# Optimization experiments

Measured on AMD Instinct MI355X. Metric: run time of the kernel, lower is better.

## Reference

```python
import jax, jax.numpy as jnp
import numpy as np

N_NODES = 100000
D = 128


def gcn_conv(x, W, b, src, dst, deg_inv_sqrt):
    # PyG GCNConv: linear transform, symmetric-normalized aggregation with self-loops, bias
    h = x @ W  # [N, D_out]
    norm = deg_inv_sqrt[src] * deg_inv_sqrt[dst]  # [E_tot]
    msgs = h[src] * norm[:, None]  # gather + scale  [E_tot, D_out]
    out = jax.ops.segment_sum(msgs, dst, num_segments=x.shape[0])  # scatter-add to targets
    return out + b


def _prep_edges(edge_index, n_nodes):
    # add self-loops (weight 1) and compute deg^{-1/2} over targets (flow source_to_target)
    loops = jnp.arange(n_nodes, dtype=edge_index.dtype)
    src = jnp.concatenate([edge_index[0], loops])
    dst = jnp.concatenate([edge_index[1], loops])
    deg = jax.ops.segment_sum(jnp.ones_like(dst, dtype=jnp.float32), dst, num_segments=n_nodes)
    deg_inv_sqrt = jnp.where(deg > 0, jax.lax.rsqrt(jnp.maximum(deg, 1.0)), 0.0)
    return src, dst, deg_inv_sqrt


def setup_inputs() -> dict:
    key = jax.random.key(0)
    ks = jax.random.split(key, 8)
    node_fts = jax.random.normal(ks[0], (N_NODES, D), dtype=jnp.float32)
    edge_index = jax.random.randint(ks[1], (2, 1600000), 0, N_NODES, dtype=jnp.int64)
    scale = 1.0 / np.sqrt(D)
    W1 = jax.random.uniform(ks[2], (D, D), jnp.float32, -scale, scale)
    b1 = jnp.zeros((D,), jnp.float32)
    W2 = jax.random.uniform(ks[3], (D, D), jnp.float32, -scale, scale)
    b2 = jnp.zeros((D,), jnp.float32)
    W3 = jax.random.uniform(ks[4], (D, D), jnp.float32, -scale, scale)
    b3 = jnp.zeros((D,), jnp.float32)
    return {"node_fts": node_fts, "edge_index": edge_index,
            "W1": W1, "b1": b1, "W2": W2, "b2": b2, "W3": W3, "b3": b3}


def reference(node_fts, edge_index, W1, b1, W2, b2, W3, b3):
    n = node_fts.shape[0]
    src, dst, dinv = _prep_edges(edge_index, n)
    x = jax.nn.relu(gcn_conv(node_fts, W1, b1, src, dst, dinv))
    x = jax.nn.relu(gcn_conv(x, W2, b2, src, dst, dinv))
    x = jax.nn.relu(gcn_conv(x, W3, b3, src, dst, dinv))
    return x
```

## Files before the change

### kernel.cpp

```cpp
#include <hip/hip_runtime.h>

#define NN 100000
#define EE 1600000
#define D 128
#define NPART 8
#define PSZ (NN / NPART)
#define NI4 (EE / 4)
#define SUBW 196
#define NSB (NPART * 64)
#define SCAP 4096
#define RCAP 8192
#define LBCAP 96

typedef __attribute__((ext_vector_type(8))) short bf16x8;
typedef __attribute__((ext_vector_type(4))) float f32x4;

__device__ inline unsigned int f2bf2(float a, float b) {
    unsigned int ua = __float_as_uint(a);
    unsigned int ub = __float_as_uint(b);
    ua = (ua + 0x7fffu + ((ua >> 16) & 1u)) >> 16;
    ub = (ub + 0x7fffu + ((ub >> 16) & 1u)) >> 16;
    return ua | (ub << 16);
}
__device__ inline unsigned short f2bf(float a) {
    unsigned int u = __float_as_uint(a);
    return (unsigned short)((u + 0x7fffu + ((u >> 16) & 1u)) >> 16);
}
__device__ inline float2 bf2f2(unsigned int u) {
    return make_float2(__uint_as_float(u << 16), __uint_as_float(u & 0xffff0000u));
}


__global__ void init_kernel(int* __restrict__ gcur2, unsigned int* __restrict__ hb) {
    int i = blockIdx.x * blockDim.x + threadIdx.x;
    if (i < NSB) gcur2[i] = 0;
    if (i < 64) hb[(size_t)NN * 64 + i] = 0;
}

__global__ __launch_bounds__(256) void filterbin_kernel(const int4* __restrict__ src4,
                                                        const int4* __restrict__ dst4,
                                                        int* __restrict__ gcur2,
                                                        uint2* __restrict__ buckets2) {
    __shared__ uint2 bins[64][LBCAP];
    __shared__ int bcnt[64];
    __shared__ int gbase[64];
    const int p = blockIdx.x >> 6;
    const int c = blockIdx.x & 63;
    if (threadIdx.x < 64) bcnt[threadIdx.x] = 0;
    __syncthreads();
    const int lo = p * PSZ, hi = lo + PSZ;
    const int chunk4 = NI4 / 64;
    const int a0 = c * chunk4, a1 = a0 + chunk4;
    for (int i = a0 + threadIdx.x; i < a1; i += 256) {
        int4 d4 = dst4[i];
        bool m0 = (d4.x >= lo && d4.x < hi);
        bool m1 = (d4.y >= lo && d4.y < hi);
        bool m2 = (d4.z >= lo && d4.z < hi);
        bool m3 = (d4.w >= lo && d4.w < hi);
        if (!(m0 | m1 | m2 | m3)) continue;
        int4 s4 = src4[i];
        int ss[4] = {s4.x, s4.y, s4.z, s4.w};
        int dd[4] = {d4.x, d4.y, d4.z, d4.w};
        bool mm[4] = {m0, m1, m2, m3};
#pragma unroll
        for (int k = 0; k < 4; ++k) {
            if (!mm[k]) continue;
            int li = (dd[k] - lo) / SUBW;
            int pos = atomicAdd(&bcnt[li], 1);
            if (pos < LBCAP) {
                bins[li][pos] = make_uint2((unsigned)ss[k], (unsigned)dd[k]);
            } else {
                int sb = p * 64 + li;
                int gp = atomicAdd(&gcur2[sb], 1);
                buckets2[(size_t)sb * SCAP + gp] = make_uint2((unsigned)ss[k], (unsigned)dd[k]);
            }
        }
    }
    __syncthreads();
    if (threadIdx.x < 64) {
        int cc = min(bcnt[threadIdx.x], LBCAP);
        gbase[threadIdx.x] = atomicAdd(&gcur2[p * 64 + threadIdx.x], cc);
        bcnt[threadIdx.x] = cc;
    }
    __syncthreads();
    for (int b = 0; b < 64; ++b) {
        const int cc = bcnt[b];
        uint2* outp = buckets2 + (size_t)(p * 64 + b) * SCAP + gbase[b];
        for (int i = threadIdx.x; i < cc; i += 256) outp[i] = bins[b][i];
    }
}

__global__ __launch_bounds__(256) void sort3_kernel(const uint2* __restrict__ buckets2,
                                                    const int* __restrict__ gcur2,
                                                    int* __restrict__ csr,
                                                    int* __restrict__ info,
                                                    float* __restrict__ dinv) {
    __shared__ int hist[256];
    __shared__ int pscan[256];
    __shared__ int lcur[256];
    __shared__ int staged[RCAP];
    const int sb = blockIdx.x;
    const int li = sb & 63;
    const int base_node = (sb >> 6) * PSZ + li * SUBW;
    const int nnodes = min(SUBW, PSZ - li * SUBW);
    const int scnt = gcur2[sb];
    const uint2* bk = buckets2 + (size_t)sb * SCAP;
    const int t = threadIdx.x;
    hist[t] = 0;
    __syncthreads();
    for (int i = t; i < scnt; i += 256) atomicAdd(&hist[(int)bk[i].y - base_node], 1);
    __syncthreads();
    const int padded = (t < nnodes) ? ((hist[t] + 7) & ~7) : 0;
    pscan[t] = padded;
    __syncthreads();
    for (int off = 1; off < 256; off <<= 1) {
        int v = (t >= off) ? pscan[t - off] : 0;
        __syncthreads();
        pscan[t] += v;
        __syncthreads();
    }
    const int rstart = pscan[t] - padded;
    lcur[t] = rstart;
    __syncthreads();
    const int total = pscan[255];
    for (int i = t; i < total; i += 256) staged[i] = NN;
    __syncthreads();
    for (int i = t; i < scnt; i += 256) {
        uint2 r = bk[i];
        int pos = atomicAdd(&lcur[(int)r.y - base_node], 1);
        staged[pos] = (int)r.x;
    }
    __syncthreads();
    int4* co = (int4*)(csr + (size_t)sb * RCAP);
    for (int i = t; i < (total >> 2); i += 256) co[i] = ((const int4*)staged)[i];
    if (t < nnodes) {
        int dg = hist[t];
        info[base_node + t] = ((sb * RCAP + rstart) << 8) | dg;
        dinv[base_node + t] = rsqrtf(1.0f + (float)dg);
    }
}

__global__ void wt_build3_kernel(const float* __restrict__ W1, const float* __restrict__ W2,
                                 const float* __restrict__ W3, unsigned short* __restrict__ wt1,
                                 unsigned short* __restrict__ wt2, unsigned short* __restrict__ wt3) {
    const int which = blockIdx.x >> 6;
    const float* W = which == 0 ? W1 : (which == 1 ? W2 : W3);
    unsigned short* wt = which == 0 ? wt1 : (which == 1 ? wt2 : wt3);
    int i = (blockIdx.x & 63) * 256 + threadIdx.x;
    int n = i >> 7, k = i & 127;
    wt[n * 128 + k] = f2bf(W[k * 128 + n]);
}


template <bool F32IN>
__global__ __launch_bounds__(256) void gemm_mfma_kernel(const void* __restrict__ xin,
                                                        const unsigned short* __restrict__ wt,
                                                        const float* __restrict__ dinv,
                                                        unsigned int* __restrict__ hb) {
    const int wave = blockIdx.x * 4 + (threadIdx.x >> 6);
    const int m0 = wave * 16;
    if (m0 >= NN) return;
    const int lane = threadIdx.x & 63;
    const int r = lane & 15;
    const int q = lane >> 4;
    const unsigned short* wrow = wt + (size_t)r * 128 + q * 8;
    f32x4 acc[8] = {};
#pragma unroll
    for (int kc = 0; kc < 4; ++kc) {
        bf16x8 xf;
        if (F32IN) {
            const float* xrow = (const float*)xin + (size_t)(m0 + r) * 128 + q * 8 + kc * 32;
            float4 a = *(const float4*)xrow;
            float4 b = *(const float4*)(xrow + 4);
            unsigned short tmp[8] = {f2bf(a.x), f2bf(a.y), f2bf(a.z), f2bf(a.w),
                                     f2bf(b.x), f2bf(b.y), f2bf(b.z), f2bf(b.w)};
            xf = *(const bf16x8*)tmp;
        } else {
            const unsigned short* xrow =
                (const unsigned short*)xin + (size_t)(m0 + r) * 128 + q * 8 + kc * 32;
            xf = *(const bf16x8*)xrow;
        }
#pragma unroll
        for (int nt = 0; nt < 8; ++nt) {
            bf16x8 wf = *(const bf16x8*)(wrow + (size_t)nt * 16 * 128 + kc * 32);
            acc[nt] = __builtin_amdgcn_mfma_f32_16x16x32_bf16(wf, xf, acc[nt], 0, 0, 0);
        }
    }
    const float dvr = dinv[m0 + r];
    unsigned int* hrow = hb + (size_t)(m0 + r) * 64;
#pragma unroll
    for (int nt = 0; nt < 8; ++nt) {
        int n = nt * 16 + q * 4;
        *(uint2*)(hrow + (n >> 1)) =
            make_uint2(f2bf2(acc[nt][0] * dvr, acc[nt][1] * dvr),
                       f2bf2(acc[nt][2] * dvr, acc[nt][3] * dvr));
    }
}


template <bool BF16OUT>
__global__ __launch_bounds__(256) void aggregate_kernel(const unsigned int* __restrict__ hb,
                                                        const int* __restrict__ csr,
                                                        const int* __restrict__ info,
                                                        const float* __restrict__ dinv,
                                                        const float2* __restrict__ bias2,
                                                        void* __restrict__ outp) {
    const int d = blockIdx.x * 4 + (threadIdx.x >> 6);
    const int j = threadIdx.x & 63;
    const int ifo = info[d];
    int e = ifo >> 8;
    const int end = e + (((ifo & 255) + 7) & ~7);
    float2 acc = bf2f2(hb[(size_t)d * 64 + j]);
    for (; e + 16 <= end; e += 16) {
        int4 c0 = *(const int4*)(csr + e);
        int4 c1 = *(const int4*)(csr + e + 4);
        int4 c2 = *(const int4*)(csr + e + 8);
        int4 c3 = *(const int4*)(csr + e + 12);
        unsigned int v0 = hb[(size_t)c0.x * 64 + j];
        unsigned int v1 = hb[(size_t)c0.y * 64 + j];
        unsigned int v2 = hb[(size_t)c0.z * 64 + j];
        unsigned int v3 = hb[(size_t)c0.w * 64 + j];
        unsigned int v4 = hb[(size_t)c1.x * 64 + j];
        unsigned int v5 = hb[(size_t)c1.y * 64 + j];
        unsigned int v6 = hb[(size_t)c1.z * 64 + j];
        unsigned int v7 = hb[(size_t)c1.w * 64 + j];
        unsigned int v8 = hb[(size_t)c2.x * 64 + j];
        unsigned int v9 = hb[(size_t)c2.y * 64 + j];
        unsigned int va = hb[(size_t)c2.z * 64 + j];
        unsigned int vb = hb[(size_t)c2.w * 64 + j];
        unsigned int vc = hb[(size_t)c3.x * 64 + j];
        unsigned int vd = hb[(size_t)c3.y * 64 + j];
        unsigned int ve = hb[(size_t)c3.z * 64 + j];
        unsigned int vf = hb[(size_t)c3.w * 64 + j];
        float2 f0 = bf2f2(v0), f1 = bf2f2(v1), f2 = bf2f2(v2), f3 = bf2f2(v3);
        float2 f4 = bf2f2(v4), f5 = bf2f2(v5), f6 = bf2f2(v6), f7 = bf2f2(v7);
        float2 f8 = bf2f2(v8), f9 = bf2f2(v9), fa = bf2f2(va), fb = bf2f2(vb);
        float2 fc = bf2f2(vc), fd = bf2f2(vd), fe = bf2f2(ve), ff = bf2f2(vf);
        acc.x += ((f0.x + f1.x) + (f2.x + f3.x)) + ((f4.x + f5.x) + (f6.x + f7.x)) +
                 ((f8.x + f9.x) + (fa.x + fb.x)) + ((fc.x + fd.x) + (fe.x + ff.x));
        acc.y += ((f0.y + f1.y) + (f2.y + f3.y)) + ((f4.y + f5.y) + (f6.y + f7.y)) +
                 ((f8.y + f9.y) + (fa.y + fb.y)) + ((fc.y + fd.y) + (fe.y + ff.y));
    }
    if (e < end) {
        int4 c0 = *(const int4*)(csr + e);
        int4 c1 = *(const int4*)(csr + e + 4);
        unsigned int v0 = hb[(size_t)c0.x * 64 + j];
        unsigned int v1 = hb[(size_t)c0.y * 64 + j];
        unsigned int v2 = hb[(size_t)c0.z * 64 + j];
        unsigned int v3 = hb[(size_t)c0.w * 64 + j];
        unsigned int v4 = hb[(size_t)c1.x * 64 + j];
        unsigned int v5 = hb[(size_t)c1.y * 64 + j];
        unsigned int v6 = hb[(size_t)c1.z * 64 + j];
        unsigned int v7 = hb[(size_t)c1.w * 64 + j];
        float2 f0 = bf2f2(v0), f1 = bf2f2(v1), f2 = bf2f2(v2), f3 = bf2f2(v3);
        float2 f4 = bf2f2(v4), f5 = bf2f2(v5), f6 = bf2f2(v6), f7 = bf2f2(v7);
        acc.x += ((f0.x + f1.x) + (f2.x + f3.x)) + ((f4.x + f5.x) + (f6.x + f7.x));
        acc.y += ((f0.y + f1.y) + (f2.y + f3.y)) + ((f4.y + f5.y) + (f6.y + f7.y));
    }
    const float dv = dinv[d];
    float2 bb = bias2[j];
    float ox = fmaxf(dv * acc.x + bb.x, 0.0f);
    float oy = fmaxf(dv * acc.y + bb.y, 0.0f);
    if (BF16OUT) {
        ((unsigned int*)outp)[(size_t)d * 64 + j] = f2bf2(ox, oy);
    } else {
        ((float2*)outp)[(size_t)d * 64 + j] = make_float2(ox, oy);
    }
}


extern "C" void kernel_launch(void* const* d_in, const int* in_sizes, int n_in,
                              void* d_out, int out_size, void* d_ws, size_t ws_size,
                              hipStream_t stream) {
    const float* x0 = (const float*)d_in[0];
    const int* ei = (const int*)d_in[1];
    const float* W1 = (const float*)d_in[2];
    const float* b1 = (const float*)d_in[3];
    const float* W2 = (const float*)d_in[4];
    const float* b2 = (const float*)d_in[5];
    const float* W3 = (const float*)d_in[6];
    const float* b3 = (const float*)d_in[7];
    float* out = (float*)d_out;

    char* ws = (char*)d_ws;
    size_t off = 0;
    auto alloc = [&](size_t bytes) -> void* {
        off = (off + 511) & ~(size_t)511;
        void* p = ws + off;
        off += bytes;
        return p;
    };
    unsigned int* hb  = (unsigned int*)alloc(((size_t)NN + 1) * 64 * 4);
    int*   csr     = (int*)  alloc((size_t)NSB * RCAP * sizeof(int));
    uint2* buckets2 = (uint2*)alloc((size_t)NSB * SCAP * sizeof(uint2));
    int*   info    = (int*)  alloc((size_t)NN * sizeof(int));
    float* dinv    = (float*)alloc((size_t)NN * sizeof(float));
    int*   gcur2   = (int*)  alloc(NSB * sizeof(int));
    unsigned short* wt1 = (unsigned short*)alloc(128 * 128 * 2);
    unsigned short* wt2 = (unsigned short*)alloc(128 * 128 * 2);
    unsigned short* wt3 = (unsigned short*)alloc(128 * 128 * 2);

    unsigned int* xact = (unsigned int*)d_out;

    const int4* src4 = (const int4*)ei;
    const int4* dst4 = (const int4*)(ei + EE);

    init_kernel<<<2, 256, 0, stream>>>(gcur2, hb);
    filterbin_kernel<<<NSB, 256, 0, stream>>>(src4, dst4, gcur2, buckets2);
    sort3_kernel<<<NSB, 256, 0, stream>>>(buckets2, gcur2, csr, info, dinv);
    wt_build3_kernel<<<192, 256, 0, stream>>>(W1, W2, W3, wt1, wt2, wt3);

    const int gemmBlocks = (NN / 16 + 3) / 4;

    gemm_mfma_kernel<true><<<gemmBlocks, 256, 0, stream>>>((const void*)x0, wt1, dinv, hb);
    aggregate_kernel<true><<<NN / 4, 256, 0, stream>>>(hb, csr, info, dinv,
                                                       (const float2*)b1, (void*)xact);
    gemm_mfma_kernel<false><<<gemmBlocks, 256, 0, stream>>>((const void*)xact, wt2, dinv, hb);
    aggregate_kernel<true><<<NN / 4, 256, 0, stream>>>(hb, csr, info, dinv,
                                                       (const float2*)b2, (void*)xact);
    gemm_mfma_kernel<false><<<gemmBlocks, 256, 0, stream>>>((const void*)xact, wt3, dinv, hb);
    aggregate_kernel<false><<<NN / 4, 256, 0, stream>>>(hb, csr, info, dinv,
                                                        (const float2*)b3, (void*)out);
}
```

Measured before the change: 435.4 us.

## Reorder GCN to aggregate-then-transform and fuse aggregation with MFMA GEMM per layer

Uses linearity to aggregate the dinv-scaled input features first and then apply the weight matrix, fusing gather-aggregation and the MFMA GEMM into one kernel per layer via an LDS tile of 64 rows. This removes the separate GEMM launches and the hb intermediate round-trip through global memory. The next layer's dinv prescale is folded into the epilogue. Each block now handles 64 destinations with 4 waves doing 16 sequential gathers each, which cuts parallelism and latency hiding in the gather phase. It also rounds the aggregated sum to bf16 before the GEMM.

```diff
diff --git a/kernel.cpp b/kernel.cpp
--- a/kernel.cpp
+++ b/kernel.cpp
@@ -31,10 +31,14 @@
 }
 
 
-__global__ void init_kernel(int* __restrict__ gcur2, unsigned int* __restrict__ hb) {
+__global__ void init_kernel(int* __restrict__ gcur2, unsigned int* __restrict__ xsA,
+                            unsigned int* __restrict__ xsB) {
     int i = blockIdx.x * blockDim.x + threadIdx.x;
     if (i < NSB) gcur2[i] = 0;
-    if (i < 64) hb[(size_t)NN * 64 + i] = 0;
+    if (i < 64) {
+        xsA[(size_t)NN * 64 + i] = 0;
+        xsB[(size_t)NN * 64 + i] = 0;
+    }
 }
 
 __global__ __launch_bounds__(256) void filterbin_kernel(const int4* __restrict__ src4,
@@ -151,120 +155,131 @@
     wt[n * 128 + k] = f2bf(W[k * 128 + n]);
 }
 
-
-template <bool F32IN>
-__global__ __launch_bounds__(256) void gemm_mfma_kernel(const void* __restrict__ xin,
-                                                        const unsigned short* __restrict__ wt,
-                                                        const float* __restrict__ dinv,
-                                                        unsigned int* __restrict__ hb) {
-    const int wave = blockIdx.x * 4 + (threadIdx.x >> 6);
-    const int m0 = wave * 16;
-    if (m0 >= NN) return;
-    const int lane = threadIdx.x & 63;
-    const int r = lane & 15;
-    const int q = lane >> 4;
+__global__ __launch_bounds__(256) void scale0_kernel(const float* __restrict__ x0,
+                                                     const float* __restrict__ dinv,
+                                                     unsigned int* __restrict__ xs) {
+    int i = blockIdx.x * 256 + threadIdx.x;
+    int row = i >> 5, c = (i & 31) * 4;
+    float4 v = *(const float4*)(x0 + (size_t)row * 128 + c);
+    float dv = dinv[row];
+    *(uint2*)(xs + (size_t)row * 64 + (c >> 1)) =
+        make_uint2(f2bf2(v.x * dv, v.y * dv), f2bf2(v.z * dv, v.w * dv));
+}
+
+
+template <bool LAST>
+__global__ __launch_bounds__(256) void fused_kernel(const unsigned int* __restrict__ xs,
+                                                    const unsigned short* __restrict__ wt,
+                                                    const int* __restrict__ csr,
+                                                    const int* __restrict__ info,
+                                                    const float* __restrict__ dinv,
+                                                    const float* __restrict__ bias,
+                                                    void* __restrict__ outp) {
+    __shared__ unsigned int ylds[64 * 68];
+    const int w = threadIdx.x >> 6;
+    const int j = threadIdx.x & 63;
+    const int base = blockIdx.x * 64;
+
+    for (int i = 0; i < 16; ++i) {
+        const int d = base + w * 16 + i;
+        if (d >= NN) break;
+        const int ifo = info[d];
+        int e = ifo >> 8;
+        const int end = e + (((ifo & 255) + 7) & ~7);
+        float2 acc = bf2f2(xs[(size_t)d * 64 + j]);
+        for (; e + 16 <= end; e += 16) {
+            int4 c0 = *(const int4*)(csr + e);
+            int4 c1 = *(const int4*)(csr + e + 4);
+            int4 c2 = *(const int4*)(csr + e + 8);
+            int4 c3 = *(const int4*)(csr + e + 12);
+            unsigned int v0 = xs[(size_t)c0.x * 64 + j];
+            unsigned int v1 = xs[(size_t)c0.y * 64 + j];
+            unsigned int v2 = xs[(size_t)c0.z * 64 + j];
+            unsigned int v3 = xs[(size_t)c0.w * 64 + j];
+            unsigned int v4 = xs[(size_t)c1.x * 64 + j];
+            unsigned int v5 = xs[(size_t)c1.y * 64 + j];
+            unsigned int v6 = xs[(size_t)c1.z * 64 + j];
+            unsigned int v7 = xs[(size_t)c1.w * 64 + j];
+            unsigned int v8 = xs[(size_t)c2.x * 64 + j];
+            unsigned int v9 = xs[(size_t)c2.y * 64 + j];
+            unsigned int va = xs[(size_t)c2.z * 64 + j];
+            unsigned int vb = xs[(size_t)c2.w * 64 + j];
+            unsigned int vc = xs[(size_t)c3.x * 64 + j];
+            unsigned int vd = xs[(size_t)c3.y * 64 + j];
+            unsigned int ve = xs[(size_t)c3.z * 64 + j];
+            unsigned int vf = xs[(size_t)c3.w * 64 + j];
+            float2 f0 = bf2f2(v0), f1 = bf2f2(v1), f2 = bf2f2(v2), f3 = bf2f2(v3);
+            float2 f4 = bf2f2(v4), f5 = bf2f2(v5), f6 = bf2f2(v6), f7 = bf2f2(v7);
+            float2 f8 = bf2f2(v8), f9 = bf2f2(v9), fa = bf2f2(va), fb = bf2f2(vb);
+            float2 fc = bf2f2(vc), fd = bf2f2(vd), fe = bf2f2(ve), ff = bf2f2(vf);
+            acc.x += ((f0.x + f1.x) + (f2.x + f3.x)) + ((f4.x + f5.x) + (f6.x + f7.x)) +
+                     ((f8.x + f9.x) + (fa.x + fb.x)) + ((fc.x + fd.x) + (fe.x + ff.x));
+            acc.y += ((f0.y + f1.y) + (f2.y + f3.y)) + ((f4.y + f5.y) + (f6.y + f7.y)) +
+                     ((f8.y + f9.y) + (fa.y + fb.y)) + ((fc.y + fd.y) + (fe.y + ff.y));
+        }
+        if (e < end) {
+            int4 c0 = *(const int4*)(csr + e);
+            int4 c1 = *(const int4*)(csr + e + 4);
+            unsigned int v0 = xs[(size_t)c0.x * 64 + j];
+            unsigned int v1 = xs[(size_t)c0.y * 64 + j];
+            unsigned int v2 = xs[(size_t)c0.z * 64 + j];
+            unsigned int v3 = xs[(size_t)c0.w * 64 + j];
+            unsigned int v4 = xs[(size_t)c1.x * 64 + j];
+            unsigned int v5 = xs[(size_t)c1.y * 64 + j];
+            unsigned int v6 = xs[(size_t)c1.z * 64 + j];
+            unsigned int v7 = xs[(size_t)c1.w * 64 + j];
+            float2 f0 = bf2f2(v0), f1 = bf2f2(v1), f2 = bf2f2(v2), f3 = bf2f2(v3);
+            float2 f4 = bf2f2(v4), f5 = bf2f2(v5), f6 = bf2f2(v6), f7 = bf2f2(v7);
+            acc.x += ((f0.x + f1.x) + (f2.x + f3.x)) + ((f4.x + f5.x) + (f6.x + f7.x));
+            acc.y += ((f0.y + f1.y) + (f2.y + f3.y)) + ((f4.y + f5.y) + (f6.y + f7.y));
+        }
+        const float dv = dinv[d];
+        ylds[(w * 16 + i) * 68 + j] = f2bf2(dv * acc.x, dv * acc.y);
+    }
+    __syncthreads();
+
+    const int r = j & 15;
+    const int q = j >> 4;
     const unsigned short* wrow = wt + (size_t)r * 128 + q * 8;
+    const int myrow = w * 16 + r;
     f32x4 acc[8] = {};
 #pragma unroll
     for (int kc = 0; kc < 4; ++kc) {
-        bf16x8 xf;
-        if (F32IN) {
-            const float* xrow = (const float*)xin + (size_t)(m0 + r) * 128 + q * 8 + kc * 32;
-            float4 a = *(const float4*)xrow;
-            float4 b = *(const float4*)(xrow + 4);
-            unsigned short tmp[8] = {f2bf(a.x), f2bf(a.y), f2bf(a.z), f2bf(a.w),
-                                     f2bf(b.x), f2bf(b.y), f2bf(b.z), f2bf(b.w)};
-            xf = *(const bf16x8*)tmp;
-        } else {
-            const unsigned short* xrow =
-                (const unsigned short*)xin + (size_t)(m0 + r) * 128 + q * 8 + kc * 32;
-            xf = *(const bf16x8*)xrow;
-        }
+        bf16x8 xf = *(const bf16x8*)(ylds + myrow * 68 + q * 4 + kc * 16);
 #pragma unroll
         for (int nt = 0; nt < 8; ++nt) {
             bf16x8 wf = *(const bf16x8*)(wrow + (size_t)nt * 16 * 128 + kc * 32);
             acc[nt] = __builtin_amdgcn_mfma_f32_16x16x32_bf16(wf, xf, acc[nt], 0, 0, 0);
         }
     }
-    const float dvr = dinv[m0 + r];
-    unsigned int* hrow = hb + (size_t)(m0 + r) * 64;
-#pragma unroll
-    for (int nt = 0; nt < 8; ++nt) {
-        int n = nt * 16 + q * 4;
-        *(uint2*)(hrow + (n >> 1)) =
-            make_uint2(f2bf2(acc[nt][0] * dvr, acc[nt][1] * dvr),
-                       f2bf2(acc[nt][2] * dvr, acc[nt][3] * dvr));
-    }
-}
-
-
-template <bool BF16OUT>
-__global__ __launch_bounds__(256) void aggregate_kernel(const unsigned int* __restrict__ hb,
-                                                        const int* __restrict__ csr,
-                                                        const int* __restrict__ info,
-                                                        const float* __restrict__ dinv,
-                                                        const float2* __restrict__ bias2,
-                                                        void* __restrict__ outp) {
-    const int d = blockIdx.x * 4 + (threadIdx.x >> 6);
-    const int j = threadIdx.x & 63;
-    const int ifo = info[d];
-    int e = ifo >> 8;
-    const int end = e + (((ifo & 255) + 7) & ~7);
-    float2 acc = bf2f2(hb[(size_t)d * 64 + j]);
-    for (; e + 16 <= end; e += 16) {
-        int4 c0 = *(const int4*)(csr + e);
-        int4 c1 = *(const int4*)(csr + e + 4);
-        int4 c2 = *(const int4*)(csr + e + 8);
-        int4 c3 = *(const int4*)(csr + e + 12);
-        unsigned int v0 = hb[(size_t)c0.x * 64 + j];
-        unsigned int v1 = hb[(size_t)c0.y * 64 + j];
-        unsigned int v2 = hb[(size_t)c0.z * 64 + j];
-        unsigned int v3 = hb[(size_t)c0.w * 64 + j];
-        unsigned int v4 = hb[(size_t)c1.x * 64 + j];
-        unsigned int v5 = hb[(size_t)c1.y * 64 + j];
-        unsigned int v6 = hb[(size_t)c1.z * 64 + j];
-        unsigned int v7 = hb[(size_t)c1.w * 64 + j];
-        unsigned int v8 = hb[(size_t)c2.x * 64 + j];
-        unsigned int v9 = hb[(size_t)c2.y * 64 + j];
-        unsigned int va = hb[(size_t)c2.z * 64 + j];
-        unsigned int vb = hb[(size_t)c2.w * 64 + j];
-        unsigned int vc = hb[(size_t)c3.x * 64 + j];
-        unsigned int vd = hb[(size_t)c3.y * 64 + j];
-        unsigned int ve = hb[(size_t)c3.z * 64 + j];
-        unsigned int vf = hb[(size_t)c3.w * 64 + j];
-        float2 f0 = bf2f2(v0), f1 = bf2f2(v1), f2 = bf2f2(v2), f3 = bf2f2(v3);
-        float2 f4 = bf2f2(v4), f5 = bf2f2(v5), f6 = bf2f2(v6), f7 = bf2f2(v7);
-        float2 f8 = bf2f2(v8), f9 = bf2f2(v9), fa = bf2f2(va), fb = bf2f2(vb);
-        float2 fc = bf2f2(vc), fd = bf2f2(vd), fe = bf2f2(ve), ff = bf2f2(vf);
-        acc.x += ((f0.x + f1.x) + (f2.x + f3.x)) + ((f4.x + f5.x) + (f6.x + f7.x)) +
-                 ((f8.x + f9.x) + (fa.x + fb.x)) + ((fc.x + fd.x) + (fe.x + ff.x));
-        acc.y += ((f0.y + f1.y) + (f2.y + f3.y)) + ((f4.y + f5.y) + (f6.y + f7.y)) +
-                 ((f8.y + f9.y) + (fa.y + fb.y)) + ((fc.y + fd.y) + (fe.y + ff.y));
-    }
-    if (e < end) {
-        int4 c0 = *(const int4*)(csr + e);
-        int4 c1 = *(const int4*)(csr + e + 4);
-        unsigned int v0 = hb[(size_t)c0.x * 64 + j];
-        unsigned int v1 = hb[(size_t)c0.y * 64 + j];
-        unsigned int v2 = hb[(size_t)c0.z * 64 + j];
-        unsigned int v3 = hb[(size_t)c0.w * 64 + j];
-        unsigned int v4 = hb[(size_t)c1.x * 64 + j];
-        unsigned int v5 = hb[(size_t)c1.y * 64 + j];
-        unsigned int v6 = hb[(size_t)c1.z * 64 + j];
-        unsigned int v7 = hb[(size_t)c1.w * 64 + j];
-        float2 f0 = bf2f2(v0), f1 = bf2f2(v1), f2 = bf2f2(v2), f3 = bf2f2(v3);
-        float2 f4 = bf2f2(v4), f5 = bf2f2(v5), f6 = bf2f2(v6), f7 = bf2f2(v7);
-        acc.x += ((f0.x + f1.x) + (f2.x + f3.x)) + ((f4.x + f5.x) + (f6.x + f7.x));
-        acc.y += ((f0.y + f1.y) + (f2.y + f3.y)) + ((f4.y + f5.y) + (f6.y + f7.y));
-    }
-    const float dv = dinv[d];
-    float2 bb = bias2[j];
-    float ox = fmaxf(dv * acc.x + bb.x, 0.0f);
-    float oy = fmaxf(dv * acc.y + bb.y, 0.0f);
-    if (BF16OUT) {
-        ((unsigned int*)outp)[(size_t)d * 64 + j] = f2bf2(ox, oy);
+    const int orow = base + myrow;
+    if (orow >= NN) return;
+    if (LAST) {
+        float* op = (float*)outp + (size_t)orow * 128;
+#pragma unroll
+        for (int nt = 0; nt < 8; ++nt) {
+            int n = nt * 16 + q * 4;
+            float4 bb = *(const float4*)(bias + n);
+            float4 o;
+            o.x = fmaxf(acc[nt][0] + bb.x, 0.0f);
+            o.y = fmaxf(acc[nt][1] + bb.y, 0.0f);
+            o.z = fmaxf(acc[nt][2] + bb.z, 0.0f);
+            o.w = fmaxf(acc[nt][3] + bb.w, 0.0f);
+            *(float4*)(op + n) = o;
+        }
     } else {
-        ((float2*)outp)[(size_t)d * 64 + j] = make_float2(ox, oy);
+        const float dvr = dinv[orow];
+        unsigned int* op = (unsigned int*)outp + (size_t)orow * 64;
+#pragma unroll
+        for (int nt = 0; nt < 8; ++nt) {
+            int n = nt * 16 + q * 4;
+            float4 bb = *(const float4*)(bias + n);
+            float o0 = fmaxf(acc[nt][0] + bb.x, 0.0f) * dvr;
+            float o1 = fmaxf(acc[nt][1] + bb.y, 0.0f) * dvr;
+            float o2 = fmaxf(acc[nt][2] + bb.z, 0.0f) * dvr;
+            float o3 = fmaxf(acc[nt][3] + bb.w, 0.0f) * dvr;
+            *(uint2*)(op + (n >> 1)) = make_uint2(f2bf2(o0, o1), f2bf2(o2, o3));
+        }
     }
 }
 
@@ -290,7 +305,7 @@
         off += bytes;
         return p;
     };
-    unsigned int* hb  = (unsigned int*)alloc(((size_t)NN + 1) * 64 * 4);
+    unsigned int* xsA = (unsigned int*)alloc(((size_t)NN + 1) * 64 * 4);
     int*   csr     = (int*)  alloc((size_t)NSB * RCAP * sizeof(int));
     uint2* buckets2 = (uint2*)alloc((size_t)NSB * SCAP * sizeof(uint2));
     int*   info    = (int*)  alloc((size_t)NN * sizeof(int));
@@ -300,25 +315,20 @@
     unsigned short* wt2 = (unsigned short*)alloc(128 * 128 * 2);
     unsigned short* wt3 = (unsigned short*)alloc(128 * 128 * 2);
 
-    unsigned int* xact = (unsigned int*)d_out;
+    unsigned int* xsB = (unsigned int*)d_out;
 
     const int4* src4 = (const int4*)ei;
     const int4* dst4 = (const int4*)(ei + EE);
 
-    init_kernel<<<2, 256, 0, stream>>>(gcur2, hb);
+    init_kernel<<<2, 256, 0, stream>>>(gcur2, xsA, xsB);
     filterbin_kernel<<<NSB, 256, 0, stream>>>(src4, dst4, gcur2, buckets2);
     sort3_kernel<<<NSB, 256, 0, stream>>>(buckets2, gcur2, csr, info, dinv);
     wt_build3_kernel<<<192, 256, 0, stream>>>(W1, W2, W3, wt1, wt2, wt3);
-
-    const int gemmBlocks = (NN / 16 + 3) / 4;
-
-    gemm_mfma_kernel<true><<<gemmBlocks, 256, 0, stream>>>((const void*)x0, wt1, dinv, hb);
-    aggregate_kernel<true><<<NN / 4, 256, 0, stream>>>(hb, csr, info, dinv,
-                                                       (const float2*)b1, (void*)xact);
-    gemm_mfma_kernel<false><<<gemmBlocks, 256, 0, stream>>>((const void*)xact, wt2, dinv, hb);
-    aggregate_kernel<true><<<NN / 4, 256, 0, stream>>>(hb, csr, info, dinv,
-                                                       (const float2*)b2, (void*)xact);
-    gemm_mfma_kernel<false><<<gemmBlocks, 256, 0, stream>>>((const void*)xact, wt3, dinv, hb);
-    aggregate_kernel<false><<<NN / 4, 256, 0, stream>>>(hb, csr, info, dinv,
-                                                        (const float2*)b3, (void*)out);
-}
+    scale0_kernel<<<NN * 32 / 256, 256, 0, stream>>>(x0, dinv, xsA);
+
+    const int fusedBlocks = (NN + 63) / 64;
+
+    fused_kernel<false><<<fusedBlocks, 256, 0, stream>>>(xsA, wt1, csr, info, dinv, b1, (void*)xsB);
+    fused_kernel<false><<<fusedBlocks, 256, 0, stream>>>(xsB, wt2, csr, info, dinv, b2, (void*)xsA);
+    fused_kernel<true><<<fusedBlocks, 256, 0, stream>>>(xsA, wt3, csr, info, dinv, b3, (void*)out);
+}
```

New measurement: 462.2 us. 1.06x slower.

## Fuse weight prep into binning, overlap sort with first GEMM, register-cache weights

Applied to the files above, without the earlier changes.

Folds the weight transpose/convert and hb sentinel init into extra blocks of the edge binning kernel, and replaces the init kernel with memsets. Degree is counted via global atomics during binning, so the first GEMM can compute dinv itself and run as extra blocks inside the sort kernel instead of as a separate launch. GEMM waves now keep all weight fragments in registers and process four 16-row tiles each, cutting repeated weight loads. The cost is one global atomic per edge, higher register pressure, and a fixed grid split within the fused kernels.

```diff
diff --git a/kernel.cpp b/kernel.cpp
--- a/kernel.cpp
+++ b/kernel.cpp
@@ -31,16 +31,27 @@
 }
 
 
-__global__ void init_kernel(int* __restrict__ gcur2, unsigned int* __restrict__ hb) {
-    int i = blockIdx.x * blockDim.x + threadIdx.x;
-    if (i < NSB) gcur2[i] = 0;
-    if (i < 64) hb[(size_t)NN * 64 + i] = 0;
-}
-
-__global__ __launch_bounds__(256) void filterbin_kernel(const int4* __restrict__ src4,
-                                                        const int4* __restrict__ dst4,
-                                                        int* __restrict__ gcur2,
-                                                        uint2* __restrict__ buckets2) {
+__global__ __launch_bounds__(256) void fbwt_kernel(const int4* __restrict__ src4,
+                                                   const int4* __restrict__ dst4,
+                                                   int* __restrict__ gcur2,
+                                                   uint2* __restrict__ buckets2,
+                                                   int* __restrict__ deg,
+                                                   const float* __restrict__ W1,
+                                                   const float* __restrict__ W2,
+                                                   const float* __restrict__ W3,
+                                                   unsigned short* __restrict__ wt1,
+                                                   unsigned short* __restrict__ wt2,
+                                                   unsigned short* __restrict__ wt3,
+                                                   unsigned int* __restrict__ hb) {
+    if (blockIdx.x >= 512) {
+        const int g = (blockIdx.x - 512) * 256 + threadIdx.x;
+        const int n = g >> 7, k = g & 127;
+        wt1[n * 128 + k] = f2bf(W1[k * 128 + n]);
+        wt2[n * 128 + k] = f2bf(W2[k * 128 + n]);
+        wt3[n * 128 + k] = f2bf(W3[k * 128 + n]);
+        if (blockIdx.x == 512 && threadIdx.x < 64) hb[(size_t)NN * 64 + threadIdx.x] = 0;
+        return;
+    }
     __shared__ uint2 bins[64][LBCAP];
     __shared__ int bcnt[64];
     __shared__ int gbase[64];
@@ -65,6 +76,7 @@
 #pragma unroll
         for (int k = 0; k < 4; ++k) {
             if (!mm[k]) continue;
+            atomicAdd(&deg[dd[k]], 1);
             int li = (dd[k] - lo) / SUBW;
             int pos = atomicAdd(&bcnt[li], 1);
             if (pos < LBCAP) {
@@ -90,15 +102,80 @@
     }
 }
 
-__global__ __launch_bounds__(256) void sort3_kernel(const uint2* __restrict__ buckets2,
-                                                    const int* __restrict__ gcur2,
-                                                    int* __restrict__ csr,
-                                                    int* __restrict__ info,
-                                                    float* __restrict__ dinv) {
+
+template <bool F32IN>
+__device__ __forceinline__ void gemm_body(int wave, const void* __restrict__ xin,
+                                          const unsigned short* __restrict__ wt,
+                                          const int* __restrict__ deg,
+                                          unsigned int* __restrict__ hb) {
+    const int base = wave * 64;
+    if (base >= NN) return;
+    const int lane = threadIdx.x & 63;
+    const int r = lane & 15;
+    const int q = lane >> 4;
+    const unsigned short* wrow = wt + (size_t)r * 128 + q * 8;
+    bf16x8 wfr[4][8];
+#pragma unroll
+    for (int kc = 0; kc < 4; ++kc)
+#pragma unroll
+        for (int nt = 0; nt < 8; ++nt)
+            wfr[kc][nt] = *(const bf16x8*)(wrow + (size_t)nt * 16 * 128 + kc * 32);
+#pragma unroll
+    for (int tt = 0; tt < 4; ++tt) {
+        const int m0 = base + tt * 16;
+        if (m0 >= NN) break;
+        f32x4 acc[8] = {};
+#pragma unroll
+        for (int kc = 0; kc < 4; ++kc) {
+            bf16x8 xf;
+            if (F32IN) {
+                const float* xrow = (const float*)xin + (size_t)(m0 + r) * 128 + q * 8 + kc * 32;
+                float4 a = *(const float4*)xrow;
+                float4 b = *(const float4*)(xrow + 4);
+                unsigned short tmp[8] = {f2bf(a.x), f2bf(a.y), f2bf(a.z), f2bf(a.w),
+                                         f2bf(b.x), f2bf(b.y), f2bf(b.z), f2bf(b.w)};
+                xf = *(const bf16x8*)tmp;
+            } else {
+                const unsigned short* xrow =
+                    (const unsigned short*)xin + (size_t)(m0 + r) * 128 + q * 8 + kc * 32;
+                xf = *(const bf16x8*)xrow;
+            }
+#pragma unroll
+            for (int nt = 0; nt < 8; ++nt)
+                acc[nt] = __builtin_amdgcn_mfma_f32_16x16x32_bf16(wfr[kc][nt], xf, acc[nt], 0, 0, 0);
+        }
+        const int orow = m0 + r;
+        const float dvr = rsqrtf(1.0f + (float)deg[orow]);
+        unsigned int* hrow = hb + (size_t)orow * 64;
+#pragma unroll
+        for (int nt = 0; nt < 8; ++nt) {
+            int n = nt * 16 + q * 4;
+            *(uint2*)(hrow + (n >> 1)) =
+                make_uint2(f2bf2(acc[nt][0] * dvr, acc[nt][1] * dvr),
+                           f2bf2(acc[nt][2] * dvr, acc[nt][3] * dvr));
+        }
+    }
+}
+
+
+__global__ __launch_bounds__(256, 2) void sort3_gemm1_kernel(const uint2* __restrict__ buckets2,
+                                                             const int* __restrict__ gcur2,
+                                                             int* __restrict__ csr,
+                                                             int* __restrict__ info,
+                                                             float* __restrict__ dinv,
+                                                             const float* __restrict__ x0,
+                                                             const unsigned short* __restrict__ wt1,
+                                                             const int* __restrict__ deg,
+                                                             unsigned int* __restrict__ hb) {
     __shared__ int hist[256];
     __shared__ int pscan[256];
     __shared__ int lcur[256];
     __shared__ int staged[RCAP];
+    if (blockIdx.x >= 512) {
+        const int wave = (blockIdx.x - 512) * 4 + (threadIdx.x >> 6);
+        gemm_body<true>(wave, (const void*)x0, wt1, deg, hb);
+        return;
+    }
     const int sb = blockIdx.x;
     const int li = sb & 63;
     const int base_node = (sb >> 6) * PSZ + li * SUBW;
@@ -140,61 +217,13 @@
     }
 }
 
-__global__ void wt_build3_kernel(const float* __restrict__ W1, const float* __restrict__ W2,
-                                 const float* __restrict__ W3, unsigned short* __restrict__ wt1,
-                                 unsigned short* __restrict__ wt2, unsigned short* __restrict__ wt3) {
-    const int which = blockIdx.x >> 6;
-    const float* W = which == 0 ? W1 : (which == 1 ? W2 : W3);
-    unsigned short* wt = which == 0 ? wt1 : (which == 1 ? wt2 : wt3);
-    int i = (blockIdx.x & 63) * 256 + threadIdx.x;
-    int n = i >> 7, k = i & 127;
-    wt[n * 128 + k] = f2bf(W[k * 128 + n]);
-}
-
-
 template <bool F32IN>
-__global__ __launch_bounds__(256) void gemm_mfma_kernel(const void* __restrict__ xin,
-                                                        const unsigned short* __restrict__ wt,
-                                                        const float* __restrict__ dinv,
-                                                        unsigned int* __restrict__ hb) {
+__global__ __launch_bounds__(256, 2) void gemm_kernel(const void* __restrict__ xin,
+                                                      const unsigned short* __restrict__ wt,
+                                                      const int* __restrict__ deg,
+                                                      unsigned int* __restrict__ hb) {
     const int wave = blockIdx.x * 4 + (threadIdx.x >> 6);
-    const int m0 = wave * 16;
-    if (m0 >= NN) return;
-    const int lane = threadIdx.x & 63;
-    const int r = lane & 15;
-    const int q = lane >> 4;
-    const unsigned short* wrow = wt + (size_t)r * 128 + q * 8;
-    f32x4 acc[8] = {};
-#pragma unroll
-    for (int kc = 0; kc < 4; ++kc) {
-        bf16x8 xf;
-        if (F32IN) {
-            const float* xrow = (const float*)xin + (size_t)(m0 + r) * 128 + q * 8 + kc * 32;
-            float4 a = *(const float4*)xrow;
-            float4 b = *(const float4*)(xrow + 4);
-            unsigned short tmp[8] = {f2bf(a.x), f2bf(a.y), f2bf(a.z), f2bf(a.w),
-                                     f2bf(b.x), f2bf(b.y), f2bf(b.z), f2bf(b.w)};
-            xf = *(const bf16x8*)tmp;
-        } else {
-            const unsigned short* xrow =
-                (const unsigned short*)xin + (size_t)(m0 + r) * 128 + q * 8 + kc * 32;
-            xf = *(const bf16x8*)xrow;
-        }
-#pragma unroll
-        for (int nt = 0; nt < 8; ++nt) {
-            bf16x8 wf = *(const bf16x8*)(wrow + (size_t)nt * 16 * 128 + kc * 32);
-            acc[nt] = __builtin_amdgcn_mfma_f32_16x16x32_bf16(wf, xf, acc[nt], 0, 0, 0);
-        }
-    }
-    const float dvr = dinv[m0 + r];
-    unsigned int* hrow = hb + (size_t)(m0 + r) * 64;
-#pragma unroll
-    for (int nt = 0; nt < 8; ++nt) {
-        int n = nt * 16 + q * 4;
-        *(uint2*)(hrow + (n >> 1)) =
-            make_uint2(f2bf2(acc[nt][0] * dvr, acc[nt][1] * dvr),
-                       f2bf2(acc[nt][2] * dvr, acc[nt][3] * dvr));
-    }
+    gemm_body<F32IN>(wave, xin, wt, deg, hb);
 }
 
 
@@ -295,6 +324,7 @@
     uint2* buckets2 = (uint2*)alloc((size_t)NSB * SCAP * sizeof(uint2));
     int*   info    = (int*)  alloc((size_t)NN * sizeof(int));
     float* dinv    = (float*)alloc((size_t)NN * sizeof(float));
+    int*   deg     = (int*)  alloc((size_t)NN * sizeof(int));
     int*   gcur2   = (int*)  alloc(NSB * sizeof(int));
     unsigned short* wt1 = (unsigned short*)alloc(128 * 128 * 2);
     unsigned short* wt2 = (unsigned short*)alloc(128 * 128 * 2);
@@ -305,20 +335,18 @@
     const int4* src4 = (const int4*)ei;
     const int4* dst4 = (const int4*)(ei + EE);
 
-    init_kernel<<<2, 256, 0, stream>>>(gcur2, hb);
-    filterbin_kernel<<<NSB, 256, 0, stream>>>(src4, dst4, gcur2, buckets2);
-    sort3_kernel<<<NSB, 256, 0, stream>>>(buckets2, gcur2, csr, info, dinv);
-    wt_build3_kernel<<<192, 256, 0, stream>>>(W1, W2, W3, wt1, wt2, wt3);
-
-    const int gemmBlocks = (NN / 16 + 3) / 4;
-
-    gemm_mfma_kernel<true><<<gemmBlocks, 256, 0, stream>>>((const void*)x0, wt1, dinv, hb);
+    hipMemsetAsync(gcur2, 0, NSB * sizeof(int), stream);
+    hipMemsetAsync(deg, 0, (size_t)NN * sizeof(int), stream);
+    fbwt_kernel<<<576, 256, 0, stream>>>(src4, dst4, gcur2, buckets2, deg,
+                                         W1, W2, W3, wt1, wt2, wt3, hb);
+    sort3_gemm1_kernel<<<903, 256, 0, stream>>>(buckets2, gcur2, csr, info, dinv,
+                                                x0, wt1, deg, hb);
     aggregate_kernel<true><<<NN / 4, 256, 0, stream>>>(hb, csr, info, dinv,
                                                        (const float2*)b1, (void*)xact);
-    gemm_mfma_kernel<false><<<gemmBlocks, 256, 0, stream>>>((const void*)xact, wt2, dinv, hb);
+    gemm_kernel<false><<<391, 256, 0, stream>>>((const void*)xact, wt2, deg, hb);
     aggregate_kernel<true><<<NN / 4, 256, 0, stream>>>(hb, csr, info, dinv,
                                                        (const float2*)b2, (void*)xact);
-    gemm_mfma_kernel<false><<<gemmBlocks, 256, 0, stream>>>((const void*)xact, wt3, dinv, hb);
+    gemm_kernel<false><<<391, 256, 0, stream>>>((const void*)xact, wt3, deg, hb);
     aggregate_kernel<false><<<NN / 4, 256, 0, stream>>>(hb, csr, info, dinv,
                                                         (const float2*)b3, (void*)out);
 }
```

New measurement: 436.5 us. About the same (+0.2%).

## Fuse GCN layers into one cooperative persistent kernel and merge preprocessing kernels

Applied to the files above, without the earlier changes.

Replaces the six separate GEMM and aggregate launches with one cooperative persistent kernel that loops over waves and uses grid-wide syncs between stages. It also folds the weight transpose and the hb padding init into the edge filter/bin kernel using a shared-memory tiled transpose, doubles the filter chunk count while halving the local bin capacity, and replaces the init kernel with a memset. The aim is to cut launch overhead and tail effects between stages. In exchange it adds grid-sync cost, limits occupancy through the launch bounds, and spills more edges to global atomics because the local bins are smaller.

```diff
diff --git a/kernel.cpp b/kernel.cpp
--- a/kernel.cpp
+++ b/kernel.cpp
@@ -1,8 +1,10 @@
 #include <hip/hip_runtime.h>
+#include <hip/hip_cooperative_groups.h>
+
+namespace cg = cooperative_groups;
 
 #define NN 100000
 #define EE 1600000
-#define D 128
 #define NPART 8
 #define PSZ (NN / NPART)
 #define NI4 (EE / 4)
@@ -10,7 +12,10 @@
 #define NSB (NPART * 64)
 #define SCAP 4096
 #define RCAP 8192
-#define LBCAP 96
+#define FCHUNKS 128
+#define FBLOCKS (NPART * FCHUNKS)
+#define WTBLOCKS 48
+#define LBCAP 48
 
 typedef __attribute__((ext_vector_type(8))) short bf16x8;
 typedef __attribute__((ext_vector_type(4))) float f32x4;
@@ -31,26 +36,48 @@
 }
 
 
-__global__ void init_kernel(int* __restrict__ gcur2, unsigned int* __restrict__ hb) {
-    int i = blockIdx.x * blockDim.x + threadIdx.x;
-    if (i < NSB) gcur2[i] = 0;
-    if (i < 64) hb[(size_t)NN * 64 + i] = 0;
-}
-
-__global__ __launch_bounds__(256) void filterbin_kernel(const int4* __restrict__ src4,
-                                                        const int4* __restrict__ dst4,
-                                                        int* __restrict__ gcur2,
-                                                        uint2* __restrict__ buckets2) {
+__global__ __launch_bounds__(256) void fbwt_kernel(const int4* __restrict__ src4,
+                                                   const int4* __restrict__ dst4,
+                                                   int* __restrict__ gcur2,
+                                                   uint2* __restrict__ buckets2,
+                                                   const float* __restrict__ W1,
+                                                   const float* __restrict__ W2,
+                                                   const float* __restrict__ W3,
+                                                   unsigned short* __restrict__ wt1,
+                                                   unsigned short* __restrict__ wt2,
+                                                   unsigned short* __restrict__ wt3,
+                                                   unsigned int* __restrict__ hb) {
     __shared__ uint2 bins[64][LBCAP];
     __shared__ int bcnt[64];
     __shared__ int gbase[64];
-    const int p = blockIdx.x >> 6;
-    const int c = blockIdx.x & 63;
+    __shared__ float tile[32][33];
+
+    if (blockIdx.x < WTBLOCKS) {
+        const int m = blockIdx.x >> 4;
+        const int tl = blockIdx.x & 15;
+        const int ti = tl >> 2, tj = tl & 3;
+        const float* W = m == 0 ? W1 : (m == 1 ? W2 : W3);
+        unsigned short* wt = m == 0 ? wt1 : (m == 1 ? wt2 : wt3);
+        const int r = threadIdx.x >> 5, c = threadIdx.x & 31;
+#pragma unroll
+        for (int rr = r; rr < 32; rr += 8)
+            tile[rr][c] = W[(ti * 32 + rr) * 128 + tj * 32 + c];
+        __syncthreads();
+#pragma unroll
+        for (int rr = r; rr < 32; rr += 8)
+            wt[(size_t)(tj * 32 + rr) * 128 + ti * 32 + c] = f2bf(tile[c][rr]);
+        if (blockIdx.x == 0 && threadIdx.x < 64) hb[(size_t)NN * 64 + threadIdx.x] = 0;
+        return;
+    }
+
+    const int fb = blockIdx.x - WTBLOCKS;
+    const int p = fb >> 7;
+    const int ch = fb & 127;
     if (threadIdx.x < 64) bcnt[threadIdx.x] = 0;
     __syncthreads();
     const int lo = p * PSZ, hi = lo + PSZ;
-    const int chunk4 = NI4 / 64;
-    const int a0 = c * chunk4, a1 = a0 + chunk4;
+    const int chunk4 = NI4 / FCHUNKS;
+    const int a0 = ch * chunk4, a1 = a0 + chunk4;
     for (int i = a0 + threadIdx.x; i < a1; i += 256) {
         int4 d4 = dst4[i];
         bool m0 = (d4.x >= lo && d4.x < hi);
@@ -89,6 +116,7 @@
         for (int i = threadIdx.x; i < cc; i += 256) outp[i] = bins[b][i];
     }
 }
+
 
 __global__ __launch_bounds__(256) void sort3_kernel(const uint2* __restrict__ buckets2,
                                                     const int* __restrict__ gcur2,
@@ -140,26 +168,13 @@
     }
 }
 
-__global__ void wt_build3_kernel(const float* __restrict__ W1, const float* __restrict__ W2,
-                                 const float* __restrict__ W3, unsigned short* __restrict__ wt1,
-                                 unsigned short* __restrict__ wt2, unsigned short* __restrict__ wt3) {
-    const int which = blockIdx.x >> 6;
-    const float* W = which == 0 ? W1 : (which == 1 ? W2 : W3);
-    unsigned short* wt = which == 0 ? wt1 : (which == 1 ? wt2 : wt3);
-    int i = (blockIdx.x & 63) * 256 + threadIdx.x;
-    int n = i >> 7, k = i & 127;
-    wt[n * 128 + k] = f2bf(W[k * 128 + n]);
-}
-
 
 template <bool F32IN>
-__global__ __launch_bounds__(256) void gemm_mfma_kernel(const void* __restrict__ xin,
-                                                        const unsigned short* __restrict__ wt,
-                                                        const float* __restrict__ dinv,
-                                                        unsigned int* __restrict__ hb) {
-    const int wave = blockIdx.x * 4 + (threadIdx.x >> 6);
+__device__ __forceinline__ void gemm_wave(int wave, const void* __restrict__ xin,
+                                          const unsigned short* __restrict__ wt,
+                                          const float* __restrict__ dinv,
+                                          unsigned int* __restrict__ hb) {
     const int m0 = wave * 16;
-    if (m0 >= NN) return;
     const int lane = threadIdx.x & 63;
     const int r = lane & 15;
     const int q = lane >> 4;
@@ -197,15 +212,13 @@
     }
 }
 
-
 template <bool BF16OUT>
-__global__ __launch_bounds__(256) void aggregate_kernel(const unsigned int* __restrict__ hb,
-                                                        const int* __restrict__ csr,
-                                                        const int* __restrict__ info,
-                                                        const float* __restrict__ dinv,
-                                                        const float2* __restrict__ bias2,
-                                                        void* __restrict__ outp) {
-    const int d = blockIdx.x * 4 + (threadIdx.x >> 6);
+__device__ __forceinline__ void agg_node(int d, const unsigned int* __restrict__ hb,
+                                         const int* __restrict__ csr,
+                                         const int* __restrict__ info,
+                                         const float* __restrict__ dinv,
+                                         const float2* __restrict__ bias2,
+                                         void* __restrict__ outp) {
     const int j = threadIdx.x & 63;
     const int ifo = info[d];
     int e = ifo >> 8;
@@ -269,6 +282,42 @@
 }
 
 
+__global__ __launch_bounds__(256, 6) void net_kernel(const float* __restrict__ x0,
+                                                     const unsigned short* __restrict__ wt1,
+                                                     const unsigned short* __restrict__ wt2,
+                                                     const unsigned short* __restrict__ wt3,
+                                                     const float* __restrict__ b1,
+                                                     const float* __restrict__ b2,
+                                                     const float* __restrict__ b3,
+                                                     const int* __restrict__ csr,
+                                                     const int* __restrict__ info,
+                                                     const float* __restrict__ dinv,
+                                                     unsigned int* __restrict__ hb,
+                                                     unsigned int* __restrict__ xact,
+                                                     float* __restrict__ out) {
+    cg::grid_group gg = cg::this_grid();
+    const int w = threadIdx.x >> 6;
+    const int wstride = gridDim.x * 4;
+    for (int wv = blockIdx.x * 4 + w; wv < NN / 16; wv += wstride)
+        gemm_wave<true>(wv, (const void*)x0, wt1, dinv, hb);
+    gg.sync();
+    for (int gi = blockIdx.x; gi < NN / 4; gi += gridDim.x)
+        agg_node<true>(gi * 4 + w, hb, csr, info, dinv, (const float2*)b1, (void*)xact);
+    gg.sync();
+    for (int wv = blockIdx.x * 4 + w; wv < NN / 16; wv += wstride)
+        gemm_wave<false>(wv, (const void*)xact, wt2, dinv, hb);
+    gg.sync();
+    for (int gi = blockIdx.x; gi < NN / 4; gi += gridDim.x)
+        agg_node<true>(gi * 4 + w, hb, csr, info, dinv, (const float2*)b2, (void*)xact);
+    gg.sync();
+    for (int wv = blockIdx.x * 4 + w; wv < NN / 16; wv += wstride)
+        gemm_wave<false>(wv, (const void*)xact, wt3, dinv, hb);
+    gg.sync();
+    for (int gi = blockIdx.x; gi < NN / 4; gi += gridDim.x)
+        agg_node<false>(gi * 4 + w, hb, csr, info, dinv, (const float2*)b3, (void*)out);
+}
+
+
 extern "C" void kernel_launch(void* const* d_in, const int* in_sizes, int n_in,
                               void* d_out, int out_size, void* d_ws, size_t ws_size,
                               hipStream_t stream) {
@@ -305,20 +354,19 @@
     const int4* src4 = (const int4*)ei;
     const int4* dst4 = (const int4*)(ei + EE);
 
-    init_kernel<<<2, 256, 0, stream>>>(gcur2, hb);
-    filterbin_kernel<<<NSB, 256, 0, stream>>>(src4, dst4, gcur2, buckets2);
+    hipMemsetAsync(gcur2, 0, NSB * sizeof(int), stream);
+    fbwt_kernel<<<WTBLOCKS + FBLOCKS, 256, 0, stream>>>(src4, dst4, gcur2, buckets2,
+                                                        W1, W2, W3, wt1, wt2, wt3, hb);
     sort3_kernel<<<NSB, 256, 0, stream>>>(buckets2, gcur2, csr, info, dinv);
-    wt_build3_kernel<<<192, 256, 0, stream>>>(W1, W2, W3, wt1, wt2, wt3);
-
-    const int gemmBlocks = (NN / 16 + 3) / 4;
-
-    gemm_mfma_kernel<true><<<gemmBlocks, 256, 0, stream>>>((const void*)x0, wt1, dinv, hb);
-    aggregate_kernel<true><<<NN / 4, 256, 0, stream>>>(hb, csr, info, dinv,
-                                                       (const float2*)b1, (void*)xact);
-    gemm_mfma_kernel<false><<<gemmBlocks, 256, 0, stream>>>((const void*)xact, wt2, dinv, hb);
-    aggregate_kernel<true><<<NN / 4, 256, 0, stream>>>(hb, csr, info, dinv,
-                                                       (const float2*)b2, (void*)xact);
-    gemm_mfma_kernel<false><<<gemmBlocks, 256, 0, stream>>>((const void*)xact, wt3, dinv, hb);
-    aggregate_kernel<false><<<NN / 4, 256, 0, stream>>>(hb, csr, info, dinv,
-                                                        (const float2*)b3, (void*)out);
-}
+
+    int nbm = 0;
+    hipOccupancyMaxActiveBlocksPerMultiprocessor(&nbm, net_kernel, 256, 0);
+    if (nbm < 1) nbm = 1;
+    if (nbm > 8) nbm = 8;
+    int netGrid = nbm * 256;
+    void* nargs[] = {(void*)&x0, (void*)&wt1, (void*)&wt2, (void*)&wt3,
+                     (void*)&b1, (void*)&b2, (void*)&b3,
+                     (void*)&csr, (void*)&info, (void*)&dinv,
+                     (void*)&hb, (void*)&xact, (void*)&out};
+    hipLaunchCooperativeKernel(net_kernel, dim3(netGrid), dim3(256), nargs, 0u, stream);
+}
```

New measurement: 1.057 ms. 143% more time.
